# Kernel tuning notes

Measured on AMD Instinct MI355X. Metric: run time of the kernel, lower is better.

## Reference

```python
import jax, jax.numpy as jnp
import numpy as np

B, S, D, H = 2, 2048, 1024, 16
HD = D // H          # head_dim = 64
HALF = HD // 2       # rotary pair count = 32


def rope_freqs(seq_len, half, base=10000.0):
    # Llama-style: theta_j = base^(-2j/head_dim), angle m*theta_j
    inv = 1.0 / (base ** (np.arange(0, half, dtype=np.float32) / half))
    ang = np.arange(seq_len, dtype=np.float32)[:, None] * inv[None, :]  # [S, half]
    return jnp.asarray(np.cos(ang)), jnp.asarray(np.sin(ang))


def setup_inputs() -> dict:
    key = jax.random.key(0)
    kx, kq, kk, kv, ko = jax.random.split(key, 5)
    cos, sin = rope_freqs(S, HALF)  # real/imag of m_theta_polar_tensor
    s = 0.02
    return {
        "x": jax.random.normal(kx, (B, S, D), dtype=jnp.float32),
        "freqs_cos": cos,
        "freqs_sin": sin,
        "Wq": jax.random.normal(kq, (D, D), dtype=jnp.float32) * s,
        "Wk": jax.random.normal(kk, (D, D), dtype=jnp.float32) * s,
        "Wv": jax.random.normal(kv, (D, D), dtype=jnp.float32) * s,
        "Wout": jax.random.normal(ko, (D, D), dtype=jnp.float32) * s,
    }


def _apply_rope(t, cos, sin):
    # t: [B, S, H, HD]; rotate consecutive pairs (complex multiply)
    b, s, h, hd = t.shape
    tr = t.reshape(b, s, h, hd // 2, 2)
    t0, t1 = tr[..., 0], tr[..., 1]
    c = cos[None, :, None, :]  # [1, S, 1, HALF]
    sn = sin[None, :, None, :]
    o0 = t0 * c - t1 * sn
    o1 = t0 * sn + t1 * c
    return jnp.stack([o0, o1], axis=-1).reshape(b, s, h, hd)


def reference(x, freqs_cos, freqs_sin, Wq, Wk, Wv, Wout):
    b, s, _ = x.shape
    q = (x @ Wq).reshape(b, s, H, HD)
    k = (x @ Wk).reshape(b, s, H, HD)
    v = (x @ Wv).reshape(b, s, H, HD)
    q = _apply_rope(q, freqs_cos, freqs_sin)
    k = _apply_rope(k, freqs_cos, freqs_sin)
    # [B, H, S, S]
    scores = jnp.einsum("bqhd,bkhd->bhqk", q, k) / jnp.sqrt(jnp.float32(HD))
    causal = jnp.triu(jnp.ones((s, s), dtype=bool), k=1)
    scores = jnp.where(causal[None, None], -jnp.inf, scores)
    weights = jax.nn.softmax(scores, axis=-1)
    vectors = jnp.einsum("bhqk,bkhd->bqhd", weights, v).reshape(b, s, D)
    return vectors @ Wout
```

## Files before the change

kernel.cpp:

```cpp
#include <hip/hip_runtime.h>
#include <stdint.h>

typedef unsigned short u16;
typedef __attribute__((ext_vector_type(8))) short short8;
typedef __attribute__((ext_vector_type(4))) short short4v;
typedef __attribute__((ext_vector_type(4))) float f32x4;
typedef __attribute__((ext_vector_type(4))) unsigned short ushort4v;
typedef __attribute__((ext_vector_type(2))) unsigned int uint2v;

#define NB 2
#define NS 2048
#define ND 1024
#define NH 16
#define HDIM 64
#define NHALF 32
#define QSCALE 0.18033688f
#define NEGBIG -3.0e38f

__device__ __forceinline__ float bf2f(u16 u) {
  union { unsigned u; float f; } v; v.u = ((unsigned)u) << 16; return v.f;
}
__device__ __forceinline__ u16 f2bf(float f) {
  union { float f; unsigned u; } v; v.f = f;
  unsigned r = v.u + 0x7fffu + ((v.u >> 16) & 1u);
  return (u16)(r >> 16);
}

__device__ __forceinline__ unsigned cvt_pk_bf16(float lo, float hi) {
  unsigned r;
  asm("v_cvt_pk_bf16_f32 %0, %1, %2" : "=v"(r) : "v"(lo), "v"(hi));
  return r;
}

__device__ __forceinline__ void gld_lds16(const u16* g, u16* l) {
  void* gv = (void*)g;
  __builtin_amdgcn_global_load_lds((__attribute__((address_space(1))) void*)gv,
                                   (__attribute__((address_space(3))) void*)l, 16, 0, 0);
}

__global__ void cvt_x(const float* __restrict__ x, u16* __restrict__ xb) {
  int i = blockIdx.x * 256 + threadIdx.x;
  float4 v = ((const float4*)x)[i];
  ushort4v o;
  o.x = f2bf(v.x); o.y = f2bf(v.y); o.z = f2bf(v.z); o.w = f2bf(v.w);
  ((ushort4v*)xb)[i] = o;
}

__global__ void transpose_w4(const float* __restrict__ W0, const float* __restrict__ W1,
                             const float* __restrict__ W2, const float* __restrict__ W3,
                             u16* __restrict__ dqkv, u16* __restrict__ dout) {
  __shared__ float tile[32][33];
  const int z = blockIdx.z;
  const float* W = (z == 0) ? W0 : (z == 1) ? W1 : (z == 2) ? W2 : W3;
  u16* dst = (z < 3) ? (dqkv + (size_t)z * ND * ND) : dout;
  const int n0 = blockIdx.x * 32, k0 = blockIdx.y * 32;
  const int tx = threadIdx.x, ty = threadIdx.y;
#pragma unroll
  for (int i = 0; i < 4; ++i)
    tile[ty + i * 8][tx] = W[(size_t)(k0 + ty + i * 8) * ND + n0 + tx];
  __syncthreads();
#pragma unroll
  for (int i = 0; i < 4; ++i)
    dst[(size_t)(n0 + ty + i * 8) * ND + k0 + tx] = f2bf(tile[tx][ty + i * 8]);
}

template<int MI, int MODE>
__global__ __launch_bounds__(256) void gemm64(
    const u16* __restrict__ A, const u16* __restrict__ BT,
    u16* __restrict__ qo, u16* __restrict__ ko, u16* __restrict__ vo,
    float* __restrict__ fo) {
  __shared__ u16 smem[MI * 2048 + 8192];
  const int tid = threadIdx.x;
  const int w = tid >> 6, lane = tid & 63;
  const int lr = lane & 15, lg = lane >> 4;
  const int bm = blockIdx.y * (MI * 32), bn = blockIdx.x << 7;
  const int wr = (w >> 1) * (MI * 16), wc = (w & 1) << 6;
  f32x4 acc[MI][4] = {};

  const int arow = tid >> 3;
  const int aslot = (tid & 7) ^ (arow & 7);
  const u16* ags = A + (size_t)(bm + arow) * ND + (aslot << 3);
  const u16* bgs = BT + (size_t)(bn + arow) * ND + (aslot << 3);
  u16* const As = smem;
  u16* const Bs = smem + MI * 2048;

  int af_off[MI][2], bf_off[4][2];
#pragma unroll
  for (int mi = 0; mi < MI; ++mi)
#pragma unroll
    for (int kk = 0; kk < 2; ++kk)
      af_off[mi][kk] = (wr + mi * 16 + lr) * 64 + ((((kk << 2) + lg) ^ (lr & 7)) << 3);
#pragma unroll
  for (int ni = 0; ni < 4; ++ni)
#pragma unroll
    for (int kk = 0; kk < 2; ++kk)
      bf_off[ni][kk] = (wc + ni * 16 + lr) * 64 + ((((kk << 2) + lg) ^ (lr & 7)) << 3);

  for (int kt = 0; kt < ND; kt += 64) {
#pragma unroll
    for (int it = 0; it < MI; ++it)
      gld_lds16(ags + it * (32 * ND) + kt, As + it * 2048 + w * 512);
#pragma unroll
    for (int it = 0; it < 4; ++it)
      gld_lds16(bgs + it * (32 * ND) + kt, Bs + it * 2048 + w * 512);
    __syncthreads();
#pragma unroll
    for (int kk = 0; kk < 2; ++kk) {
      short8 af[MI], bfr[4];
#pragma unroll
      for (int mi = 0; mi < MI; ++mi)
        af[mi] = *(const short8*)(As + af_off[mi][kk]);
#pragma unroll
      for (int ni = 0; ni < 4; ++ni)
        bfr[ni] = *(const short8*)(Bs + bf_off[ni][kk]);
#pragma unroll
      for (int mi = 0; mi < MI; ++mi)
#pragma unroll
        for (int ni = 0; ni < 4; ++ni)
          acc[mi][ni] = __builtin_amdgcn_mfma_f32_16x16x32_bf16(af[mi], bfr[ni], acc[mi][ni], 0, 0, 0);
    }
    __syncthreads();
  }

  if (MODE == 0) {
#pragma unroll
    for (int mi = 0; mi < MI; ++mi) {
#pragma unroll
      for (int ni = 0; ni < 4; ++ni) {
        const int n = bn + wc + ni * 16 + lr;
        const int which = n >> 10, hh = (n >> 6) & 15, d = n & 63;
        if (which == 2) {
          const int m0 = bm + wr + mi * 16 + (lg << 2);
          const int b = m0 >> 11, s0 = m0 & 2047;
          uint2v pk;
          pk.x = cvt_pk_bf16(acc[mi][ni][0], acc[mi][ni][1]);
          pk.y = cvt_pk_bf16(acc[mi][ni][2], acc[mi][ni][3]);
          *(uint2v*)(vo + ((size_t)(b * NH + hh) * HDIM + d) * NS + s0) = pk;
        } else {
          u16* dst = which == 0 ? qo : ko;
#pragma unroll
          for (int j = 0; j < 4; ++j) {
            const int m = bm + wr + mi * 16 + (lg << 2) + j;
            const int b = m >> 11, s = m & 2047;
            dst[(((size_t)(b * NH + hh) * NS + s) << 6) + d] = f2bf(acc[mi][ni][j]);
          }
        }
      }
    }
  } else {
#pragma unroll
    for (int mi = 0; mi < MI; ++mi)
#pragma unroll
      for (int ni = 0; ni < 4; ++ni)
#pragma unroll
        for (int j = 0; j < 4; ++j) {
          const int m = bm + wr + mi * 16 + (lg << 2) + j;
          const int n = bn + wc + ni * 16 + lr;
          fo[(size_t)m * ND + n] = acc[mi][ni][j];
        }
  }
}

__global__ void rope_k(u16* __restrict__ Qb, u16* __restrict__ Kb,
                       const float* __restrict__ cosT, const float* __restrict__ sinT) {
  int t = blockIdx.x * 256 + threadIdx.x;
  int g = t & 7;
  int s = (t >> 3) & 2047;
  int bh = t >> 14;
  float4 c4 = *(const float4*)(cosT + s * NHALF + (g << 2));
  float4 s4 = *(const float4*)(sinT + s * NHALF + (g << 2));
  size_t off = (((size_t)bh * NS + s) << 6) + (g << 3);
  short8 q = *(const short8*)(Qb + off);
  short8 k = *(const short8*)(Kb + off);
  float cc[4] = {c4.x, c4.y, c4.z, c4.w}, ss[4] = {s4.x, s4.y, s4.z, s4.w};
  short8 qo, ko;
#pragma unroll
  for (int p = 0; p < 4; ++p) {
    float q0 = bf2f((u16)q[2 * p]), q1 = bf2f((u16)q[2 * p + 1]);
    qo[2 * p]     = (short)f2bf((q0 * cc[p] - q1 * ss[p]) * QSCALE);
    qo[2 * p + 1] = (short)f2bf((q0 * ss[p] + q1 * cc[p]) * QSCALE);
    float k0 = bf2f((u16)k[2 * p]), k1 = bf2f((u16)k[2 * p + 1]);
    ko[2 * p]     = (short)f2bf(k0 * cc[p] - k1 * ss[p]);
    ko[2 * p + 1] = (short)f2bf(k0 * ss[p] + k1 * cc[p]);
  }
  *(short8*)(Qb + off) = qo;
  *(short8*)(Kb + off) = ko;
}

__global__ __launch_bounds__(256, 4) void attn_k(
    const u16* __restrict__ Qb, const u16* __restrict__ Kb,
    const u16* __restrict__ VT, u16* __restrict__ Ob) {
  __shared__ u16 K2[2][4096];
  __shared__ u16 V2[2][4096];
  __shared__ u16 Pl[4][1024];
  const int tid = threadIdx.x, w = tid >> 6, lane = tid & 63;
  const int lr = lane & 15, lg = lane >> 4;
  const int bid = blockIdx.x;
  const int xcd = bid & 7, i = bid >> 3;
  const int bh = xcd * 4 + (i & 3);
  const int pair = i >> 2;
  const int b = bh >> 4, h = bh & 15;
  const u16* Qp = Qb + (size_t)bh * NS * HDIM;
  const u16* Kp = Kb + (size_t)bh * NS * HDIM;
  const u16* Vp = VT + (size_t)bh * NS * HDIM;

  int kf_off[4][2], vb_off[4][2], pw_off[4], pa_off[2];
#pragma unroll
  for (int u = 0; u < 4; ++u) {
    const int kvr = (u << 4) + lr;
#pragma unroll
    for (int c = 0; c < 2; ++c)
      kf_off[u][c] = kvr * 64 + ((((c << 6) + (lg << 4)) ^ ((kvr & 7) << 4)) >> 1);
  }
#pragma unroll
  for (int dn = 0; dn < 4; ++dn) {
    const int d = (dn << 4) + lr;
#pragma unroll
    for (int ks = 0; ks < 2; ++ks)
      vb_off[dn][ks] = d * 64 + ((((ks << 6) + (lg << 4)) ^ ((d & 7) << 4)) >> 1);
  }
#pragma unroll
  for (int u = 0; u < 4; ++u)
    pw_off[u] = lr * 64 + ((((u << 5) + (lg << 3)) ^ ((lr & 7) << 4)) >> 1);
#pragma unroll
  for (int ks = 0; ks < 2; ++ks)
    pa_off[ks] = lr * 64 + ((((ks << 6) + (lg << 4)) ^ ((lr & 7) << 4)) >> 1);
  u16* Pw = &Pl[w][0];

  const int rr = tid >> 3, slot = tid & 7;
  const int soff = (((slot << 4) ^ ((rr & 7) << 4)) >> 1);
  const u16* kg0 = Kp + rr * HDIM + soff;
  const u16* kg1 = Kp + (rr + 32) * HDIM + soff;
  const u16* vg0 = Vp + (size_t)rr * NS + soff;
  const u16* vg1 = Vp + (size_t)(rr + 32) * NS + soff;

#define STAGE(BUFI, KV0)                                         \
  {                                                              \
    gld_lds16(kg0 + (KV0) * HDIM, &K2[BUFI][w * 512]);           \
    gld_lds16(kg1 + (KV0) * HDIM, &K2[BUFI][(4 + w) * 512]);     \
    gld_lds16(vg0 + (KV0),        &V2[BUFI][w * 512]);           \
    gld_lds16(vg1 + (KV0),        &V2[BUFI][(4 + w) * 512]);     \
  }

#define STEP(BUF, KVT)                                                            \
  {                                                                               \
    const int kv0 = (KVT) << 6;                                                   \
    if ((KVT) + 1 < nst) STAGE(BUF ^ 1, kv0 + 64);                                \
    const u16* Kl = K2[BUF];                                                      \
    const u16* Vl = V2[BUF];                                                      \
    f32x4 st[4] = {};                                                             \
    __builtin_amdgcn_s_setprio(1);                                                \
    _Pragma("unroll") for (int u = 0; u < 4; ++u)                                 \
      _Pragma("unroll") for (int c = 0; c < 2; ++c)                               \
        st[u] = __builtin_amdgcn_mfma_f32_16x16x32_bf16(                          \
            *(const short8*)(Kl + kf_off[u][c]), qf[c], st[u], 0, 0, 0);          \
    __builtin_amdgcn_s_setprio(0);                                                \
    if (kv0 + 63 > qw) {                                                          \
      _Pragma("unroll") for (int u = 0; u < 4; ++u)                               \
        _Pragma("unroll") for (int j = 0; j < 4; ++j) {                           \
          const int kvg = kv0 + (u << 4) + (lg << 2) + j;                         \
          if (kvg > q_col) st[u][j] = NEGBIG;                                     \
        }                                                                         \
    }                                                                             \
    _Pragma("unroll") for (int u = 0; u < 4; ++u) {                               \
      const float e0 = __builtin_amdgcn_exp2f(st[u][0]);                          \
      const float e1 = __builtin_amdgcn_exp2f(st[u][1]);                          \
      const float e2 = __builtin_amdgcn_exp2f(st[u][2]);                          \
      const float e3 = __builtin_amdgcn_exp2f(st[u][3]);                          \
      lacc += (e0 + e1) + (e2 + e3);                                              \
      uint2v pk;                                                                  \
      pk.x = cvt_pk_bf16(e0, e1);                                                 \
      pk.y = cvt_pk_bf16(e2, e3);                                                 \
      *(uint2v*)(Pw + pw_off[u]) = pk;                                            \
    }                                                                             \
    {                                                                             \
      short8 pa0 = *(const short8*)(Pw + pa_off[0]);                              \
      short8 pa1 = *(const short8*)(Pw + pa_off[1]);                              \
      __builtin_amdgcn_s_setprio(1);                                              \
      _Pragma("unroll") for (int dn = 0; dn < 4; ++dn) {                          \
        o[dn] = __builtin_amdgcn_mfma_f32_16x16x32_bf16(                          \
            pa0, *(const short8*)(Vl + vb_off[dn][0]), o[dn], 0, 0, 0);           \
        o[dn] = __builtin_amdgcn_mfma_f32_16x16x32_bf16(                          \
            pa1, *(const short8*)(Vl + vb_off[dn][1]), o[dn], 0, 0, 0);           \
      }                                                                           \
      __builtin_amdgcn_s_setprio(0);                                              \
    }                                                                             \
    __syncthreads();                                                              \
  }

  for (int seg = 0; seg < 2; ++seg) {
    const int tile = seg ? pair : 31 - pair;
    const int q0 = tile << 6;
    const int qw = q0 + w * 16;
    const int q_col = qw + lr;
    const int nst = tile + 1;

    short8 qf[2];
#pragma unroll
    for (int c = 0; c < 2; ++c)
      qf[c] = *(const short8*)(Qp + (size_t)(qw + lr) * HDIM + c * 32 + lg * 8);

    f32x4 o[4] = {};
    float lacc = 0.f;

    STAGE(0, 0);
    __syncthreads();

    int kvt = 0;
    for (; kvt + 2 <= nst; kvt += 2) {
      STEP(0, kvt);
      STEP(1, kvt + 1);
    }
    if (kvt < nst) STEP(0, kvt);

    float rs = lacc;
    rs += __shfl_xor(rs, 16);
    rs += __shfl_xor(rs, 32);
    float li[4];
#pragma unroll
    for (int j = 0; j < 4; ++j) li[j] = 1.0f / __shfl(rs, (lg << 2) + j);
#pragma unroll
    for (int dn = 0; dn < 4; ++dn)
#pragma unroll
      for (int j = 0; j < 4; ++j) {
        const int m = b * NS + qw + (lg << 2) + j;
        const int col = h * 64 + dn * 16 + lr;
        Ob[(size_t)m * ND + col] = f2bf(o[dn][j] * li[j]);
      }
  }
}

extern "C" void kernel_launch(void* const* d_in, const int* in_sizes, int n_in,
                              void* d_out, int out_size, void* d_ws, size_t ws_size,
                              hipStream_t stream) {
  const float* x  = (const float*)d_in[0];
  const float* fc = (const float*)d_in[1];
  const float* fs = (const float*)d_in[2];
  const float* Wq = (const float*)d_in[3];
  const float* Wk = (const float*)d_in[4];
  const float* Wv = (const float*)d_in[5];
  const float* Wo = (const float*)d_in[6];
  float* out = (float*)d_out;
  char* ws = (char*)d_ws;

  u16* xb    = (u16*)(ws);
  u16* Ob    = (u16*)(ws);
  u16* WTqkv = (u16*)(ws + (size_t)(8u << 20));
  u16* WTo   = (u16*)(ws + (size_t)(14u << 20));
  u16* Qb    = (u16*)(ws + (size_t)(16u << 20));
  u16* Kb    = (u16*)(ws + (size_t)(24u << 20));
  u16* VT    = (u16*)(ws + (size_t)(32u << 20));

  cvt_x<<<4096, 256, 0, stream>>>(x, xb);
  transpose_w4<<<dim3(32, 32, 4), dim3(32, 8), 0, stream>>>(Wq, Wk, Wv, Wo, WTqkv, WTo);
  gemm64<4, 0><<<dim3(24, 32), 256, 0, stream>>>(xb, WTqkv, Qb, Kb, VT, nullptr);
  rope_k<<<2048, 256, 0, stream>>>(Qb, Kb, fc, fs);
  attn_k<<<512, 256, 0, stream>>>(Qb, Kb, VT, Ob);
  gemm64<2, 1><<<dim3(8, 64), 256, 0, stream>>>(Ob, WTo, nullptr, nullptr, nullptr, out);
}
```

Before: 114.3 us.

## Fuse RoPE into QK projection epilogue and double-buffer GEMM LDS staging

The separate rope_k kernel is removed. RoPE rotation and the Q scale are now applied in the QKV GEMM epilogue, using swapped MFMA operands so each lane holds consecutive head-dim pairs and can write packed bf16. The QKV GEMM is split into a Q/K launch and a separate V launch that keeps the transposed layout. The GEMM k-loop now double-buffers shared memory so the next tile's global-to-LDS load is issued before the current tile's MFMAs. This removes a full read-modify-write pass over Q and K, at the cost of doubled LDS per block (which may lower occupancy) and one extra kernel launch.

```diff
diff --git a/kernel.cpp b/kernel.cpp
--- a/kernel.cpp
+++ b/kernel.cpp
@@ -3,7 +3,6 @@
 
 typedef unsigned short u16;
 typedef __attribute__((ext_vector_type(8))) short short8;
-typedef __attribute__((ext_vector_type(4))) short short4v;
 typedef __attribute__((ext_vector_type(4))) float f32x4;
 typedef __attribute__((ext_vector_type(4))) unsigned short ushort4v;
 typedef __attribute__((ext_vector_type(2))) unsigned int uint2v;
@@ -68,8 +67,9 @@
 __global__ __launch_bounds__(256) void gemm64(
     const u16* __restrict__ A, const u16* __restrict__ BT,
     u16* __restrict__ qo, u16* __restrict__ ko, u16* __restrict__ vo,
-    float* __restrict__ fo) {
-  __shared__ u16 smem[MI * 2048 + 8192];
+    float* __restrict__ fo,
+    const float* __restrict__ cosT, const float* __restrict__ sinT) {
+  __shared__ u16 smem[2][MI * 2048 + 8192];
   const int tid = threadIdx.x;
   const int w = tid >> 6, lane = tid & 63;
   const int lr = lane & 15, lg = lane >> 4;
@@ -81,8 +81,6 @@
   const int aslot = (tid & 7) ^ (arow & 7);
   const u16* ags = A + (size_t)(bm + arow) * ND + (aslot << 3);
   const u16* bgs = BT + (size_t)(bn + arow) * ND + (aslot << 3);
-  u16* const As = smem;
-  u16* const Bs = smem + MI * 2048;
 
   int af_off[MI][2], bf_off[4][2];
 #pragma unroll
@@ -96,14 +94,23 @@
     for (int kk = 0; kk < 2; ++kk)
       bf_off[ni][kk] = (wc + ni * 16 + lr) * 64 + ((((kk << 2) + lg) ^ (lr & 7)) << 3);
 
+#define GSTAGE(BUF, KT)                                                     \
+  {                                                                         \
+    _Pragma("unroll")                                                       \
+    for (int it = 0; it < MI; ++it)                                         \
+      gld_lds16(ags + it * (32 * ND) + (KT), &smem[BUF][it * 2048 + w * 512]); \
+    _Pragma("unroll")                                                       \
+    for (int it = 0; it < 4; ++it)                                          \
+      gld_lds16(bgs + it * (32 * ND) + (KT), &smem[BUF][MI * 2048 + it * 2048 + w * 512]); \
+  }
+
+  GSTAGE(0, 0);
+  __syncthreads();
+  int cur = 0;
   for (int kt = 0; kt < ND; kt += 64) {
-#pragma unroll
-    for (int it = 0; it < MI; ++it)
-      gld_lds16(ags + it * (32 * ND) + kt, As + it * 2048 + w * 512);
-#pragma unroll
-    for (int it = 0; it < 4; ++it)
-      gld_lds16(bgs + it * (32 * ND) + kt, Bs + it * 2048 + w * 512);
-    __syncthreads();
+    if (kt + 64 < ND) GSTAGE(cur ^ 1, kt + 64);
+    const u16* As = smem[cur];
+    const u16* Bs = smem[cur] + MI * 2048;
 #pragma unroll
     for (int kk = 0; kk < 2; ++kk) {
       short8 af[MI], bfr[4];
@@ -116,35 +123,53 @@
 #pragma unroll
       for (int mi = 0; mi < MI; ++mi)
 #pragma unroll
-        for (int ni = 0; ni < 4; ++ni)
-          acc[mi][ni] = __builtin_amdgcn_mfma_f32_16x16x32_bf16(af[mi], bfr[ni], acc[mi][ni], 0, 0, 0);
+        for (int ni = 0; ni < 4; ++ni) {
+          if (MODE == 0)
+            acc[mi][ni] = __builtin_amdgcn_mfma_f32_16x16x32_bf16(bfr[ni], af[mi], acc[mi][ni], 0, 0, 0);
+          else
+            acc[mi][ni] = __builtin_amdgcn_mfma_f32_16x16x32_bf16(af[mi], bfr[ni], acc[mi][ni], 0, 0, 0);
+        }
     }
     __syncthreads();
+    cur ^= 1;
   }
 
   if (MODE == 0) {
+#pragma unroll
+    for (int mi = 0; mi < MI; ++mi) {
+      const int m = bm + wr + mi * 16 + lr;
+      const int b = m >> 11, s = m & 2047;
+      const float* cbase = cosT + s * NHALF;
+      const float* sbase = sinT + s * NHALF;
+#pragma unroll
+      for (int ni = 0; ni < 4; ++ni) {
+        const int n = bn + wc + ni * 16 + (lg << 2);
+        const int which = n >> 10, hh = (n >> 6) & 15, d0 = n & 63;
+        u16* dst = which == 0 ? qo : ko;
+        const float sc = which == 0 ? QSCALE : 1.0f;
+        const float2 cp = *(const float2*)(cbase + (d0 >> 1));
+        const float2 sp = *(const float2*)(sbase + (d0 >> 1));
+        const float v0 = acc[mi][ni][0], v1 = acc[mi][ni][1];
+        const float v2 = acc[mi][ni][2], v3 = acc[mi][ni][3];
+        uint2v pk;
+        pk.x = cvt_pk_bf16((v0 * cp.x - v1 * sp.x) * sc, (v0 * sp.x + v1 * cp.x) * sc);
+        pk.y = cvt_pk_bf16((v2 * cp.y - v3 * sp.y) * sc, (v2 * sp.y + v3 * cp.y) * sc);
+        *(uint2v*)(dst + (((size_t)(b * NH + hh) * NS + s) << 6) + d0) = pk;
+      }
+    }
+  } else if (MODE == 1) {
 #pragma unroll
     for (int mi = 0; mi < MI; ++mi) {
 #pragma unroll
       for (int ni = 0; ni < 4; ++ni) {
         const int n = bn + wc + ni * 16 + lr;
-        const int which = n >> 10, hh = (n >> 6) & 15, d = n & 63;
-        if (which == 2) {
-          const int m0 = bm + wr + mi * 16 + (lg << 2);
-          const int b = m0 >> 11, s0 = m0 & 2047;
-          uint2v pk;
-          pk.x = cvt_pk_bf16(acc[mi][ni][0], acc[mi][ni][1]);
-          pk.y = cvt_pk_bf16(acc[mi][ni][2], acc[mi][ni][3]);
-          *(uint2v*)(vo + ((size_t)(b * NH + hh) * HDIM + d) * NS + s0) = pk;
-        } else {
-          u16* dst = which == 0 ? qo : ko;
-#pragma unroll
-          for (int j = 0; j < 4; ++j) {
-            const int m = bm + wr + mi * 16 + (lg << 2) + j;
-            const int b = m >> 11, s = m & 2047;
-            dst[(((size_t)(b * NH + hh) * NS + s) << 6) + d] = f2bf(acc[mi][ni][j]);
-          }
-        }
+        const int hh = n >> 6, d = n & 63;
+        const int m0 = bm + wr + mi * 16 + (lg << 2);
+        const int b = m0 >> 11, s0 = m0 & 2047;
+        uint2v pk;
+        pk.x = cvt_pk_bf16(acc[mi][ni][0], acc[mi][ni][1]);
+        pk.y = cvt_pk_bf16(acc[mi][ni][2], acc[mi][ni][3]);
+        *(uint2v*)(vo + ((size_t)(b * NH + hh) * HDIM + d) * NS + s0) = pk;
       }
     }
   } else {
@@ -159,32 +184,6 @@
           fo[(size_t)m * ND + n] = acc[mi][ni][j];
         }
   }
-}
-
-__global__ void rope_k(u16* __restrict__ Qb, u16* __restrict__ Kb,
-                       const float* __restrict__ cosT, const float* __restrict__ sinT) {
-  int t = blockIdx.x * 256 + threadIdx.x;
-  int g = t & 7;
-  int s = (t >> 3) & 2047;
-  int bh = t >> 14;
-  float4 c4 = *(const float4*)(cosT + s * NHALF + (g << 2));
-  float4 s4 = *(const float4*)(sinT + s * NHALF + (g << 2));
-  size_t off = (((size_t)bh * NS + s) << 6) + (g << 3);
-  short8 q = *(const short8*)(Qb + off);
-  short8 k = *(const short8*)(Kb + off);
-  float cc[4] = {c4.x, c4.y, c4.z, c4.w}, ss[4] = {s4.x, s4.y, s4.z, s4.w};
-  short8 qo, ko;
-#pragma unroll
-  for (int p = 0; p < 4; ++p) {
-    float q0 = bf2f((u16)q[2 * p]), q1 = bf2f((u16)q[2 * p + 1]);
-    qo[2 * p]     = (short)f2bf((q0 * cc[p] - q1 * ss[p]) * QSCALE);
-    qo[2 * p + 1] = (short)f2bf((q0 * ss[p] + q1 * cc[p]) * QSCALE);
-    float k0 = bf2f((u16)k[2 * p]), k1 = bf2f((u16)k[2 * p + 1]);
-    ko[2 * p]     = (short)f2bf(k0 * cc[p] - k1 * ss[p]);
-    ko[2 * p + 1] = (short)f2bf(k0 * ss[p] + k1 * cc[p]);
-  }
-  *(short8*)(Qb + off) = qo;
-  *(short8*)(Kb + off) = ko;
 }
 
 __global__ __launch_bounds__(256, 4) void attn_k(
@@ -350,11 +349,12 @@
   u16* Qb    = (u16*)(ws + (size_t)(16u << 20));
   u16* Kb    = (u16*)(ws + (size_t)(24u << 20));
   u16* VT    = (u16*)(ws + (size_t)(32u << 20));
+  u16* WTv   = WTqkv + (size_t)2 * ND * ND;
 
   cvt_x<<<4096, 256, 0, stream>>>(x, xb);
   transpose_w4<<<dim3(32, 32, 4), dim3(32, 8), 0, stream>>>(Wq, Wk, Wv, Wo, WTqkv, WTo);
-  gemm64<4, 0><<<dim3(24, 32), 256, 0, stream>>>(xb, WTqkv, Qb, Kb, VT, nullptr);
-  rope_k<<<2048, 256, 0, stream>>>(Qb, Kb, fc, fs);
+  gemm64<4, 0><<<dim3(16, 32), 256, 0, stream>>>(xb, WTqkv, Qb, Kb, nullptr, nullptr, fc, fs);
+  gemm64<4, 1><<<dim3(8, 32), 256, 0, stream>>>(xb, WTv, nullptr, nullptr, VT, nullptr, nullptr, nullptr);
   attn_k<<<512, 256, 0, stream>>>(Qb, Kb, VT, Ob);
-  gemm64<2, 1><<<dim3(8, 64), 256, 0, stream>>>(Ob, WTo, nullptr, nullptr, nullptr, out);
-}
+  gemm64<2, 2><<<dim3(8, 64), 256, 0, stream>>>(Ob, WTo, nullptr, nullptr, nullptr, out, nullptr, nullptr);
+}
```

Result: faster. 109.1 us (-4.5%).
